# Kernel optimization log

Measured on AMD Instinct MI355X. Metric: run time of the kernel, lower is better.

The kernel has to match this reference:

```python
import jax, jax.numpy as jnp
import numpy as np

N = 8_388_608
C = 3  # 3 sentiment classes; |argmax - y| == 2 <=> class-0/class-2 confusion


def setup_inputs() -> dict:
    key = jax.random.key(0)
    k1, k2 = jax.random.split(key)
    logits = jax.random.normal(k1, (N, C), dtype=jnp.float32)
    # original module expects log-softmax outputs
    pre = jax.nn.log_softmax(logits, axis=-1)
    y_true = jax.random.randint(k2, (N,), 0, C, dtype=jnp.int64)
    weight = jnp.float32(2.0)
    return {"pre": pre, "y_true": y_true, "weight": weight}


def reference(pre, y_true, weight):
    # gather log-prob of true class: pre[i, y_true[i]]
    picked = jnp.take_along_axis(pre, y_true[:, None], axis=1)[:, 0]  # [N]
    pred = jnp.argmax(pre, axis=-1)                                   # [N]
    # penalize opposite-polarity mistakes (|pred - y| == 2)
    penal = jnp.abs(pred - y_true) == 2                               # [N] bool
    w = jnp.where(penal, weight, jnp.float32(1.0))                    # [N]
    return -jnp.sum(w * picked) / jnp.float32(pre.shape[0])
```

## Files before the change

kernel.cpp:

```cpp
#include <hip/hip_runtime.h>


#define N_ROWS   8388608
#define NGROUPS  (N_ROWS / 4)
#define GRID     2048
#define BLOCK    256
#define NTHREADS (GRID * BLOCK)

__device__ __forceinline__ float row4(const float4& a, const float4& b, const float4& c,
                                      const int4& yy, float wgt) {
    const float r[12] = {a.x, a.y, a.z, a.w, b.x, b.y, b.z, b.w, c.x, c.y, c.z, c.w};
    const int   yi[4] = {yy.x, yy.y, yy.z, yy.w};
    float acc = 0.0f;
    #pragma unroll
    for (int k = 0; k < 4; ++k) {
        const float p0 = r[3 * k + 0];
        const float p1 = r[3 * k + 1];
        const float p2 = r[3 * k + 2];
        const int   t  = yi[k];
        const float picked = (t == 0) ? p0 : ((t == 1) ? p1 : p2);
        int pred = 0;
        float m = p0;
        if (p1 > m) { m = p1; pred = 1; }
        if (p2 > m) { pred = 2; }
        const bool penal = (pred - t == 2) || (t - pred == 2);
        acc += (penal ? wgt : 1.0f) * picked;
    }
    return acc;
}

__global__ __launch_bounds__(BLOCK) void nll_fused_kernel(
        const float* __restrict__ pre,
        const int*   __restrict__ y_true,
        const float* __restrict__ wptr,
        float*       __restrict__ out) {
    const float wgt = wptr[0];
    const float4* __restrict__ pre4 = (const float4*)pre;
    const int4*   __restrict__ y4   = (const int4*)y_true;

    const int tid = blockIdx.x * BLOCK + threadIdx.x;
    const int g0 = tid;
    const int g1 = tid + NTHREADS;
    const int g2 = tid + 2 * NTHREADS;
    const int g3 = tid + 3 * NTHREADS;

    float4 a0 = pre4[3 * g0 + 0], b0 = pre4[3 * g0 + 1], c0 = pre4[3 * g0 + 2];
    float4 a1 = pre4[3 * g1 + 0], b1 = pre4[3 * g1 + 1], c1 = pre4[3 * g1 + 2];
    float4 a2 = pre4[3 * g2 + 0], b2 = pre4[3 * g2 + 1], c2 = pre4[3 * g2 + 2];
    float4 a3 = pre4[3 * g3 + 0], b3 = pre4[3 * g3 + 1], c3 = pre4[3 * g3 + 2];
    int4 y0 = y4[g0], y1 = y4[g1], y2 = y4[g2], y3 = y4[g3];

    float acc = 0.0f;
    acc += row4(a0, b0, c0, y0, wgt);
    acc += row4(a1, b1, c1, y1, wgt);
    acc += row4(a2, b2, c2, y2, wgt);
    acc += row4(a3, b3, c3, y3, wgt);

    #pragma unroll
    for (int off = 32; off > 0; off >>= 1)
        acc += __shfl_down(acc, off, 64);

    __shared__ float smem[BLOCK / 64];
    const int lane = threadIdx.x & 63;
    const int wave = threadIdx.x >> 6;
    if (lane == 0) smem[wave] = acc;
    __syncthreads();

    if (threadIdx.x == 0) {
        float s = smem[0] + smem[1] + smem[2] + smem[3];
        atomicAdd(out, s * (-1.0f / (float)N_ROWS));
    }
}

extern "C" void kernel_launch(void* const* d_in, const int* in_sizes, int n_in,
                              void* d_out, int out_size, void* d_ws, size_t ws_size,
                              hipStream_t stream) {
    const float* pre  = (const float*)d_in[0];
    const int*   y    = (const int*)d_in[1];
    const float* wptr = (const float*)d_in[2];
    float* out = (float*)d_out;

    nll_fused_kernel<<<GRID, BLOCK, 0, stream>>>(pre, y, wptr, out);
}
```

Before: 172.9 us.

## Stage logits through shared memory with block-contiguous coalesced loads

Each block now handles a contiguous chunk of 2048 rows. It loads that chunk's logits with fully coalesced float4 reads, one per thread per stride, and the labels as scalar coalesced reads. The logits are transposed through a 24 KB LDS tile so each thread then reads its 3 row values from shared memory. The grid grows to 4096 blocks with 8 rows per thread. This is meant to improve global access contiguity, at the cost of LDS traffic, a barrier, and possible LDS bank conflicts from the stride-3 reads.

```diff
diff --git a/kernel.cpp b/kernel.cpp
--- a/kernel.cpp
+++ b/kernel.cpp
@@ -2,72 +2,67 @@
 
 
 #define N_ROWS   8388608
-#define NGROUPS  (N_ROWS / 4)
-#define GRID     2048
 #define BLOCK    256
-#define NTHREADS (GRID * BLOCK)
-
-__device__ __forceinline__ float row4(const float4& a, const float4& b, const float4& c,
-                                      const int4& yy, float wgt) {
-    const float r[12] = {a.x, a.y, a.z, a.w, b.x, b.y, b.z, b.w, c.x, c.y, c.z, c.w};
-    const int   yi[4] = {yy.x, yy.y, yy.z, yy.w};
-    float acc = 0.0f;
-    #pragma unroll
-    for (int k = 0; k < 4; ++k) {
-        const float p0 = r[3 * k + 0];
-        const float p1 = r[3 * k + 1];
-        const float p2 = r[3 * k + 2];
-        const int   t  = yi[k];
-        const float picked = (t == 0) ? p0 : ((t == 1) ? p1 : p2);
-        int pred = 0;
-        float m = p0;
-        if (p1 > m) { m = p1; pred = 1; }
-        if (p2 > m) { pred = 2; }
-        const bool penal = (pred - t == 2) || (t - pred == 2);
-        acc += (penal ? wgt : 1.0f) * picked;
-    }
-    return acc;
-}
+#define RPT      8
+#define RPB      (BLOCK * RPT)
+#define GRID     (N_ROWS / RPB)
+#define F4PT     (RPB * 3 / 4 / BLOCK)
 
 __global__ __launch_bounds__(BLOCK) void nll_fused_kernel(
         const float* __restrict__ pre,
         const int*   __restrict__ y_true,
         const float* __restrict__ wptr,
         float*       __restrict__ out) {
+    __shared__ float tile[RPB * 3];
+    __shared__ float red[BLOCK / 64];
+
     const float wgt = wptr[0];
-    const float4* __restrict__ pre4 = (const float4*)pre;
-    const int4*   __restrict__ y4   = (const int4*)y_true;
+    const int   t   = threadIdx.x;
+    const int   rowBase = (int)blockIdx.x * RPB;
+    const float4* __restrict__ pre4 = (const float4*)pre + (rowBase * 3) / 4;
+    const int*    __restrict__ yb   = y_true + rowBase;
 
-    const int tid = blockIdx.x * BLOCK + threadIdx.x;
-    const int g0 = tid;
-    const int g1 = tid + NTHREADS;
-    const int g2 = tid + 2 * NTHREADS;
-    const int g3 = tid + 3 * NTHREADS;
+    float4 v[F4PT];
+    #pragma unroll
+    for (int i = 0; i < F4PT; ++i) v[i] = pre4[t + BLOCK * i];
 
-    float4 a0 = pre4[3 * g0 + 0], b0 = pre4[3 * g0 + 1], c0 = pre4[3 * g0 + 2];
-    float4 a1 = pre4[3 * g1 + 0], b1 = pre4[3 * g1 + 1], c1 = pre4[3 * g1 + 2];
-    float4 a2 = pre4[3 * g2 + 0], b2 = pre4[3 * g2 + 1], c2 = pre4[3 * g2 + 2];
-    float4 a3 = pre4[3 * g3 + 0], b3 = pre4[3 * g3 + 1], c3 = pre4[3 * g3 + 2];
-    int4 y0 = y4[g0], y1 = y4[g1], y2 = y4[g2], y3 = y4[g3];
+    int yv[RPT];
+    #pragma unroll
+    for (int j = 0; j < RPT; ++j) yv[j] = yb[t + BLOCK * j];
+
+    float4* tile4 = (float4*)tile;
+    #pragma unroll
+    for (int i = 0; i < F4PT; ++i) tile4[t + BLOCK * i] = v[i];
+    __syncthreads();
 
     float acc = 0.0f;
-    acc += row4(a0, b0, c0, y0, wgt);
-    acc += row4(a1, b1, c1, y1, wgt);
-    acc += row4(a2, b2, c2, y2, wgt);
-    acc += row4(a3, b3, c3, y3, wgt);
+    #pragma unroll
+    for (int j = 0; j < RPT; ++j) {
+        const int r = t + BLOCK * j;
+        const float p0 = tile[3 * r + 0];
+        const float p1 = tile[3 * r + 1];
+        const float p2 = tile[3 * r + 2];
+        const int   tt = yv[j];
+        const float picked = (tt == 0) ? p0 : ((tt == 1) ? p1 : p2);
+        int pred = 0;
+        float m = p0;
+        if (p1 > m) { m = p1; pred = 1; }
+        if (p2 > m) { pred = 2; }
+        const bool penal = (pred - tt == 2) || (tt - pred == 2);
+        acc += (penal ? wgt : 1.0f) * picked;
+    }
 
     #pragma unroll
     for (int off = 32; off > 0; off >>= 1)
         acc += __shfl_down(acc, off, 64);
 
-    __shared__ float smem[BLOCK / 64];
-    const int lane = threadIdx.x & 63;
-    const int wave = threadIdx.x >> 6;
-    if (lane == 0) smem[wave] = acc;
+    const int lane = t & 63;
+    const int wave = t >> 6;
+    if (lane == 0) red[wave] = acc;
     __syncthreads();
 
-    if (threadIdx.x == 0) {
-        float s = smem[0] + smem[1] + smem[2] + smem[3];
+    if (t == 0) {
+        float s = red[0] + red[1] + red[2] + red[3];
         atomicAdd(out, s * (-1.0f / (float)N_ROWS));
     }
 }
```

Result: slower. 187.6 us (+8.5%).
